# Kernel tuning notes

Hardware: AMD Instinct MI355X
Metric: run time of the kernel (lower is better)

The kernel has to match this reference:

```python
import jax, jax.numpy as jnp
import numpy as np

MARGIN = 0.075
CONF_THRESHOLD = 0.2


def setup_inputs() -> dict:
    key = jax.random.key(0)
    k1, k2, k3 = jax.random.split(key, 3)
    N, D = 32768, 256
    embeddings = jax.random.normal(k1, (N, D), dtype=jnp.float32)
    tags = jax.random.randint(k2, (N,), 0, 500, dtype=jnp.int64)
    confidences = jax.random.uniform(k3, (N,), dtype=jnp.float32)
    return {"embeddings": embeddings, "tags": tags, "confidences": confidences}


def _safe_sqrt(sq):
    # gradient-safe sqrt: zero at sq<=0 (matches d(0)=0, avoids NaN in vjp)
    pos = sq > 0
    return jnp.where(pos, jnp.sqrt(jnp.where(pos, sq, 1.0)), 0.0)


def _triplet_hard_mining(emb, labels):
    n = emb.shape[0]
    # pairwise euclidean distances (cdist p=2)
    sq_norm = jnp.sum(emb * emb, axis=1)  # [n]
    sq = sq_norm[:, None] + sq_norm[None, :] - 2.0 * (emb @ emb.T)
    dist = _safe_sqrt(jnp.maximum(sq, 0.0))  # [n, n]

    same = labels[:, None] == labels[None, :]
    eye = jnp.eye(n, dtype=bool)
    pos_mask = same & ~eye
    neg_mask = ~same

    inf = jnp.float32(jnp.inf)
    hard_pos = jnp.max(jnp.where(pos_mask, dist, -inf), axis=1)  # [n]
    neg_min = jnp.min(jnp.where(neg_mask, dist, inf), axis=1)    # [n]
    # semi-hard negatives: neg dists strictly greater than hardest positive
    shn_mask = neg_mask & (dist > hard_pos[:, None])
    shn_min = jnp.min(jnp.where(shn_mask, dist, inf), axis=1)
    hard_neg = jnp.where(jnp.isfinite(shn_min), shn_min, neg_min)

    valid = jnp.any(pos_mask, axis=1) & jnp.any(neg_mask, axis=1)
    per_anchor = jax.nn.relu(hard_pos - hard_neg + MARGIN)
    per_anchor = jnp.where(valid, per_anchor, 0.0)
    cnt = jnp.sum(valid.astype(jnp.float32))
    # if no valid anchors (also covers <2 unique labels), loss is 0
    return jnp.where(cnt > 0, jnp.sum(per_anchor) / jnp.maximum(cnt, 1.0), 0.0)


def reference(embeddings, tags, confidences):
    n = embeddings.shape[0]
    top_k = int(CONF_THRESHOLD * n)
    _, idx = jax.lax.top_k(confidences, top_k)
    emb = embeddings[idx]
    labels = tags[idx]
    return _triplet_hard_mining(emb, labels)
```

## Files before the change

kernel.cpp:

```cpp
#include <hip/hip_runtime.h>
#include <math.h>

#define D 256
#define MARGIN 0.075f
#define MAXM 96

typedef __bf16 bf8_t __attribute__((ext_vector_type(8)));
typedef float f4_t __attribute__((ext_vector_type(4)));
typedef unsigned long long ull;

#define AS1 __attribute__((address_space(1)))
#define AS3 __attribute__((address_space(3)))
static __device__ __forceinline__ void gload_lds16(const void* g, void* s) {
    __builtin_amdgcn_global_load_lds((const AS1 unsigned int*)g, (AS3 unsigned int*)s, 16, 0, 0);
}

static __device__ __forceinline__ unsigned short f2bf(float x) {
    unsigned u = __float_as_uint(x);
    unsigned r = (u + 0x7fffu + ((u >> 16) & 1u)) >> 16;
    return (unsigned short)r;
}

static __device__ __forceinline__ float dec_min(unsigned cm) {
    return (cm == 0u) ? __builtin_inff() : __uint_as_float(~cm);
}

static __device__ __forceinline__ float rmin16(float v) {
    int s;
    s = __builtin_amdgcn_update_dpp(__float_as_int(v), __float_as_int(v), 0x101, 0xF, 0xF, false);
    v = fminf(v, __int_as_float(s));
    s = __builtin_amdgcn_update_dpp(__float_as_int(v), __float_as_int(v), 0x102, 0xF, 0xF, false);
    v = fminf(v, __int_as_float(s));
    s = __builtin_amdgcn_update_dpp(__float_as_int(v), __float_as_int(v), 0x104, 0xF, 0xF, false);
    v = fminf(v, __int_as_float(s));
    s = __builtin_amdgcn_update_dpp(__float_as_int(v), __float_as_int(v), 0x108, 0xF, 0xF, false);
    v = fminf(v, __int_as_float(s));
    return v;
}

__global__ void k_hist1(const float* __restrict__ conf, int n,
                        unsigned* __restrict__ hist) {
    int i = blockIdx.x * blockDim.x + threadIdx.x;
    if (i < n) atomicAdd(&hist[__float_as_uint(conf[i]) >> 16], 1u);
}

__global__ __launch_bounds__(1024) void k_scan(const unsigned* __restrict__ hist,
                                               unsigned* __restrict__ ctrl, int ksel) {
    __shared__ unsigned part[1024];
    __shared__ int schunk;
    int t = threadIdx.x;
    unsigned k = (unsigned)ksel;
    unsigned s = 0;
    const uint4* h4 = (const uint4*)(hist + t * 64);
    #pragma unroll
    for (int b = 0; b < 16; b++) { uint4 v = h4[b]; s += v.x + v.y + v.z + v.w; }
    part[t] = s;
    __syncthreads();
    for (int off = 1; off < 1024; off <<= 1) {
        unsigned v = (t + off < 1024) ? part[t + off] : 0u;
        __syncthreads();
        part[t] += v;
        __syncthreads();
    }
    if (part[t] >= k && (t == 1023 || part[t + 1] < k)) schunk = t;
    __syncthreads();
    if (t == 0) {
        int c = schunk;
        unsigned cum = (c == 1023) ? 0u : part[c + 1];
        int bin = 0; unsigned rem = 1;
        for (int b = 63; b >= 0; b--) {
            unsigned h = hist[c * 64 + b];
            if (cum + h >= k) { bin = c * 64 + b; rem = k - cum; break; }
            cum += h;
        }
        ctrl[3] = (unsigned)bin;
        ctrl[1] = k - rem;
        ctrl[2] = rem;
    }
}

__global__ void k_sel(const float* __restrict__ conf, int n,
                      unsigned* __restrict__ ctrl, int* __restrict__ idx_sel,
                      ull* __restrict__ cand) {
    int i = blockIdx.x * blockDim.x + threadIdx.x;
    if (i < n) {
        unsigned u = __float_as_uint(conf[i]);
        unsigned t16 = u >> 16, b16 = ctrl[3];
        if (t16 > b16) {
            unsigned pos = atomicAdd(&ctrl[5], 1u);
            idx_sel[pos] = i;
        } else if (t16 == b16) {
            unsigned pos = atomicAdd(&ctrl[6], 1u);
            cand[pos] = ((ull)u << 32) | (unsigned)i;
        }
    }
}

__global__ __launch_bounds__(256) void k_sel2(const unsigned* __restrict__ ctrl,
                                              const ull* __restrict__ cand,
                                              int* __restrict__ idx_sel) {
    int t = threadIdx.x;
    int M = (int)ctrl[6];
    unsigned need = ctrl[2], cgt = ctrl[1];
    for (int j = t; j < M; j += 256) {
        ull cj = cand[j];
        unsigned uj = (unsigned)(cj >> 32);
        unsigned rank = 0;
        for (int m = 0; m < M; m++) {
            ull cm = cand[m];
            unsigned um = (unsigned)(cm >> 32);
            if (um > uj || (um == uj && cm < cj)) rank++;
        }
        if (rank < need) idx_sel[cgt + rank] = (int)(unsigned)(cj & 0xFFFFFFFFu);
    }
}

__global__ void k_gather(const float* __restrict__ emb, const int* __restrict__ tags,
                         const int* __restrict__ idx_sel, int ksel, int np,
                         unsigned short* __restrict__ ebf, float* __restrict__ sqn,
                         int* __restrict__ lsel, unsigned* __restrict__ labhist,
                         int* __restrict__ members) {
    int j = blockIdx.x;
    int t = threadIdx.x;
    if (j < ksel) {
        int src = idx_sel[j];
        float4 v = *(const float4*)&emb[(size_t)src * D + t * 4];
        ushort4 o;
        o.x = f2bf(v.x); o.y = f2bf(v.y); o.z = f2bf(v.z); o.w = f2bf(v.w);
        *(ushort4*)&ebf[(size_t)j * D + t * 4] = o;
        float s = v.x * v.x + v.y * v.y + v.z * v.z + v.w * v.w;
        for (int off = 32; off > 0; off >>= 1) s += __shfl_down(s, off);
        if (t == 0) {
            int lab = tags[src];
            sqn[j] = s; lsel[j] = lab;
            unsigned slot = atomicAdd(&labhist[lab], 1u);
            if (slot < MAXM) members[lab * MAXM + slot] = j;
        }
    } else {
        ushort4 z = {0, 0, 0, 0};
        *(ushort4*)&ebf[(size_t)j * D + t * 4] = z;
        if (t == 0) { sqn[j] = 0.f; lsel[j] = -1; }
    }
}

__global__ __launch_bounds__(256) void k_hardpos(const unsigned short* __restrict__ ebf,
                                                 const float* __restrict__ sqn,
                                                 const int* __restrict__ members,
                                                 const unsigned* __restrict__ labhist,
                                                 unsigned* __restrict__ hp_g) {
    int L = blockIdx.x;
    int t = threadIdx.x;
    int m = (int)labhist[L];
    if (m > MAXM) m = MAXM;
    if (m < 2) return;

    __shared__ unsigned short rows[MAXM * 256];
    __shared__ float lsqn[MAXM];
    __shared__ unsigned hpl[MAXM];
    __shared__ int ridx[MAXM];

    for (int a = t; a < m; a += 256) {
        int r = members[L * MAXM + a];
        ridx[a] = r; lsqn[a] = sqn[r]; hpl[a] = 0u;
    }
    __syncthreads();
    for (int e = t * 8; e < m * 256; e += 256 * 8) {
        int a = e >> 8, c = e & 255;
        *(uint4*)&rows[a * 256 + c] = *(const uint4*)&ebf[(size_t)ridx[a] * D + c];
    }
    __syncthreads();

    int npair = m * (m - 1) / 2;
    for (int pidx = t; pidx < npair; pidx += 256) {
        int a = 0, rem = pidx;
        while (rem >= m - 1 - a) { rem -= m - 1 - a; a++; }
        int b = a + 1 + rem;
        const unsigned* ra = (const unsigned*)&rows[a * 256];
        const unsigned* rb = (const unsigned*)&rows[b * 256];
        float dot = 0.f;
        #pragma unroll 8
        for (int c = 0; c < 128; c++) {
            unsigned ua = ra[c], ub = rb[c];
            float a0 = __uint_as_float(ua << 16);
            float a1 = __uint_as_float(ua & 0xFFFF0000u);
            float b0 = __uint_as_float(ub << 16);
            float b1 = __uint_as_float(ub & 0xFFFF0000u);
            dot = fmaf(a0, b0, dot);
            dot = fmaf(a1, b1, dot);
        }
        float dsq = fmaxf(lsqn[a] + lsqn[b] - 2.f * dot, 0.f);
        unsigned bits = __float_as_uint(dsq);
        atomicMax(&hpl[a], bits);
        atomicMax(&hpl[b], bits);
    }
    __syncthreads();
    for (int a = t; a < m; a += 256) hp_g[ridx[a]] = hpl[a];
}

__global__ __launch_bounds__(256, 3) void k_fused(const unsigned short* __restrict__ Ebf,
                                                  const float* __restrict__ sqn,
                                                  const int* __restrict__ lsel,
                                                  const unsigned* __restrict__ hp_g,
                                                  unsigned* __restrict__ nm_g,
                                                  unsigned* __restrict__ shn_g,
                                                  int np, int nb, int ksel) {
    int rem = blockIdx.x, bi = 0;
    while (rem >= nb - bi) { rem -= nb - bi; bi++; }
    int bj = bi + rem;
    int i0 = bi * 128, j0 = bj * 128;
    bool diag = (bi == bj);

    __shared__ __align__(16) char smem[32768];
    char* ldsA = smem;
    char* ldsB = smem + 16384;

    int t = threadIdx.x;
    int w = t >> 6, l = t & 63;
    int wm = w & 1, wn = w >> 1;
    int lr = l & 15, lq = l >> 4;
    int r7 = lr & 7, rh = lr >> 3;

    int dr = l >> 3;
    int sg = (l & 7) ^ dr;
    const unsigned short* gA = Ebf + (size_t)(i0 + dr) * D + sg * 8;
    const unsigned short* gB = Ebf + (size_t)(j0 + dr) * D + sg * 8;

    f4_t zero = {0.f, 0.f, 0.f, 0.f};
    f4_t acc[4][4];
    #pragma unroll
    for (int p = 0; p < 4; p++)
        #pragma unroll
        for (int q = 0; q < 4; q++) acc[p][q] = zero;

    for (int k0 = 0; k0 < D; k0 += 64) {
        #pragma unroll
        for (int c = 0; c < 4; c++) {
            int R0 = w * 32 + c * 8;
            gload_lds16(gA + (size_t)R0 * D + k0, ldsA + R0 * 128);
            gload_lds16(gB + (size_t)R0 * D + k0, ldsB + R0 * 128);
        }
        __syncthreads();
        #pragma unroll
        for (int ks8 = 0; ks8 < 8; ks8 += 4) {
            bf8_t a[4], b[4];
            #pragma unroll
            for (int p = 0; p < 4; p++) {
                int off = ((wm * 8 + p * 2 + rh) << 10) + ((r7 * 8 + ((ks8 + lq) ^ r7)) << 4);
                a[p] = *(const bf8_t*)(ldsA + off);
            }
            #pragma unroll
            for (int q = 0; q < 4; q++) {
                int off = ((wn * 8 + q * 2 + rh) << 10) + ((r7 * 8 + ((ks8 + lq) ^ r7)) << 4);
                b[q] = *(const bf8_t*)(ldsB + off);
            }
            #pragma unroll
            for (int p = 0; p < 4; p++)
                #pragma unroll
                for (int q = 0; q < 4; q++)
                    acc[p][q] = __builtin_amdgcn_mfma_f32_16x16x32_bf16(a[p], b[q], acc[p][q], 0, 0, 0);
        }
        __syncthreads();
    }

    float* sqnA = (float*)smem;
    float* sqnB = sqnA + 128;
    int* labA = (int*)(sqnB + 128);
    int* labB = labA + 128;
    float* hpA2 = (float*)(labB + 128);
    float* hpB2 = hpA2 + 128;
    if (t < 128) {
        sqnA[t] = sqn[i0 + t];
        labA[t] = lsel[i0 + t];
        hpA2[t] = __uint_as_float(hp_g[i0 + t]);
    } else {
        int u = t - 128;
        sqnB[u] = sqn[j0 + u];
        labB[u] = lsel[j0 + u];
        hpB2[u] = __uint_as_float(hp_g[j0 + u]);
    }
    __syncthreads();

    const float INF = __builtin_inff();
    float dsq[4][4][4];
    int colL[4], ljv[4];
    #pragma unroll
    for (int q = 0; q < 4; q++) { colL[q] = wn * 64 + q * 16 + lr; ljv[q] = labB[colL[q]]; }
    #pragma unroll
    for (int p = 0; p < 4; p++) {
        #pragma unroll
        for (int r = 0; r < 4; r++) {
            int rowL = wm * 64 + p * 16 + lq * 4 + r;
            int gm = i0 + rowL;
            float smi = sqnA[rowL];
            #pragma unroll
            for (int q = 0; q < 4; q++) {
                int gn = j0 + colL[q];
                float s = fmaxf(smi + sqnB[colL[q]] - 2.f * acc[p][q][r], 0.f);
                dsq[p][q][r] = (gm < ksel && gn < ksel) ? s : INF;
            }
        }
    }

    #pragma unroll
    for (int p = 0; p < 4; p++) {
        #pragma unroll
        for (int r = 0; r < 4; r++) {
            int rowL = wm * 64 + p * 16 + lq * 4 + r;
            int li = labA[rowL];
            float hpr = hpA2[rowL];
            float nmv = INF, smv = INF;
            #pragma unroll
            for (int q = 0; q < 4; q++) {
                float d = dsq[p][q][r];
                if (ljv[q] != li) {
                    nmv = fminf(nmv, d);
                    if (d > hpr) smv = fminf(smv, d);
                }
            }
            nmv = rmin16(nmv);
            smv = rmin16(smv);
            if (lr == 0) {
                if (nmv < INF) atomicMax(&nm_g[i0 + rowL], ~__float_as_uint(nmv));
                if (smv < INF) atomicMax(&shn_g[i0 + rowL], ~__float_as_uint(smv));
            }
        }
    }

    if (!diag) {
        #pragma unroll
        for (int q = 0; q < 4; q++) {
            int lj = ljv[q];
            float hpc = hpB2[colL[q]];
            float nmv = INF, smv = INF;
            #pragma unroll
            for (int p = 0; p < 4; p++)
                #pragma unroll
                for (int r = 0; r < 4; r++) {
                    int rowL = wm * 64 + p * 16 + lq * 4 + r;
                    float d = dsq[p][q][r];
                    if (labA[rowL] != lj) {
                        nmv = fminf(nmv, d);
                        if (d > hpc) smv = fminf(smv, d);
                    }
                }
            nmv = fminf(nmv, __shfl_xor(nmv, 16));
            nmv = fminf(nmv, __shfl_xor(nmv, 32));
            smv = fminf(smv, __shfl_xor(smv, 16));
            smv = fminf(smv, __shfl_xor(smv, 32));
            if (lq == 0) {
                if (nmv < INF) atomicMax(&nm_g[j0 + colL[q]], ~__float_as_uint(nmv));
                if (smv < INF) atomicMax(&shn_g[j0 + colL[q]], ~__float_as_uint(smv));
            }
        }
    }
}

__global__ __launch_bounds__(256) void k_loss(const unsigned* __restrict__ hp,
                                              const unsigned* __restrict__ nm,
                                              const unsigned* __restrict__ shn,
                                              const int* __restrict__ lsel,
                                              const unsigned* __restrict__ labhist,
                                              int ksel, float* __restrict__ fsums,
                                              unsigned* __restrict__ ctrl,
                                              float* __restrict__ out) {
    __shared__ float ssum[256], scnt[256];
    int t = threadIdx.x;
    int i = blockIdx.x * 256 + t;
    float sum = 0.f, cnt = 0.f;
    if (i < ksel) {
        int li = lsel[i];
        unsigned h = labhist[li];
        bool valid = (h >= 2u) && ((unsigned)ksel > h);
        float hp2 = __uint_as_float(hp[i]);
        float nm2 = dec_min(nm[i]);
        float sh2 = dec_min(shn[i]);
        float hn2 = isinf(sh2) ? nm2 : sh2;
        float lv = valid ? fmaxf(sqrtf(hp2) - sqrtf(hn2) + MARGIN, 0.f) : 0.f;
        sum = lv;
        cnt = valid ? 1.f : 0.f;
    }
    ssum[t] = sum; scnt[t] = cnt;
    __syncthreads();
    for (int off = 128; off > 0; off >>= 1) {
        if (t < off) { ssum[t] += ssum[t + off]; scnt[t] += scnt[t + off]; }
        __syncthreads();
    }
    if (t == 0) {
        atomicAdd(&fsums[0], ssum[0]);
        atomicAdd(&fsums[1], scnt[0]);
        __threadfence();
        unsigned done = atomicAdd(&ctrl[7], 1u);
        if (done == gridDim.x - 1) {
            float s = atomicAdd(&fsums[0], 0.f);
            float c = atomicAdd(&fsums[1], 0.f);
            out[0] = (c > 0.f) ? (s / fmaxf(c, 1.f)) : 0.f;
        }
    }
}

__global__ void k_wsfail(float* out, float code) { out[0] = code; }

static inline size_t align_up(size_t x, size_t a) { return (x + a - 1) & ~(a - 1); }

extern "C" void kernel_launch(void* const* d_in, const int* in_sizes, int n_in,
                              void* d_out, int out_size, void* d_ws, size_t ws_size,
                              hipStream_t stream) {
    const float* emb  = (const float*)d_in[0];
    const int*   tags = (const int*)d_in[1];
    const float* conf = (const float*)d_in[2];
    float* out = (float*)d_out;

    int n = in_sizes[2];
    int ksel = (int)(0.2 * (double)n);
    int np = ((ksel + 127) / 128) * 128;
    int nb = np / 128;
    int nlab = 512;

    size_t off = 0;
    size_t o_ctrl = off; off = align_up(off + 32 * sizeof(unsigned), 256);
    size_t o_fs   = off; off = align_up(off + 8 * sizeof(float), 256);
    size_t o_lh   = off; off = align_up(off + (size_t)nlab * 4, 256);
    size_t o_hp   = off; off = align_up(off + (size_t)np * 4, 256);
    size_t o_nm   = off; off = align_up(off + (size_t)np * 4, 256);
    size_t o_shn  = off; off = align_up(off + (size_t)np * 4, 256);
    size_t o_h1   = off; off = align_up(off + 65536 * 4, 256);
    size_t zero_bytes = off;
    size_t o_idx  = off; off = align_up(off + (size_t)ksel * 4, 256);
    size_t o_cand = off; off = align_up(off + (size_t)n * 8, 256);
    size_t o_mem  = off; off = align_up(off + (size_t)nlab * MAXM * 4, 256);
    size_t o_lab  = off; off = align_up(off + (size_t)np * 4, 256);
    size_t o_sqn  = off; off = align_up(off + (size_t)np * 4, 256);
    size_t o_ebf  = off; off = align_up(off + (size_t)np * D * 2, 256);

    if (ws_size < off) {
        k_wsfail<<<1, 1, 0, stream>>>(out, -(float)(ws_size >> 20));
        return;
    }

    char* ws = (char*)d_ws;
    unsigned*       ctrl    = (unsigned*)(ws + o_ctrl);
    float*          fsums   = (float*)(ws + o_fs);
    unsigned*       labhist = (unsigned*)(ws + o_lh);
    unsigned*       hp_g    = (unsigned*)(ws + o_hp);
    unsigned*       nm_g    = (unsigned*)(ws + o_nm);
    unsigned*       shn_g   = (unsigned*)(ws + o_shn);
    unsigned*       h1      = (unsigned*)(ws + o_h1);
    int*            idx_sel = (int*)(ws + o_idx);
    ull*            cand    = (ull*)(ws + o_cand);
    int*            members = (int*)(ws + o_mem);
    int*            lsel    = (int*)(ws + o_lab);
    float*          sqn     = (float*)(ws + o_sqn);
    unsigned short* ebf     = (unsigned short*)(ws + o_ebf);

    hipMemsetAsync(d_ws, 0, zero_bytes, stream);
    k_hist1<<<(n + 255) / 256, 256, 0, stream>>>(conf, n, h1);
    k_scan<<<1, 1024, 0, stream>>>(h1, ctrl, ksel);
    k_sel<<<(n + 255) / 256, 256, 0, stream>>>(conf, n, ctrl, idx_sel, cand);
    k_sel2<<<1, 256, 0, stream>>>(ctrl, cand, idx_sel);
    k_gather<<<np, 64, 0, stream>>>(emb, tags, idx_sel, ksel, np, ebf, sqn, lsel,
                                    labhist, members);
    k_hardpos<<<512, 256, 0, stream>>>(ebf, sqn, members, labhist, hp_g);
    int ntri = nb * (nb + 1) / 2;
    k_fused<<<ntri, 256, 0, stream>>>(ebf, sqn, lsel, hp_g, nm_g, shn_g, np, nb, ksel);
    k_loss<<<(ksel + 255) / 256, 256, 0, stream>>>(hp_g, nm_g, shn_g, lsel, labhist,
                                                   ksel, fsums, ctrl, out);
}
```

Measured before the change: 186.2 us.

## Fuse selection kernels via last-block pattern, double-buffer GEMM tiles, fold loss into fused kernel

Merges the histogram and scan kernels, and the select and rank kernels, into single launches where the last block to finish does the serial tail work. The histogram shrinks to a smaller bin range with clamping, and the rank pass stages candidates in LDS. The loss reduction is folded into the end of the pairwise-distance kernel through a last-block counter. The tile loop of the distance GEMM now double-buffers its K tiles in 64KB of LDS, with occupancy lowered from 3 to 2. Padding rows use an infinite squared norm so per-element bounds checks can be dropped. The aim is to cut launch count and idle gaps, at the cost of serial last-block tails and lower occupancy.

```diff
diff --git a/kernel.cpp b/kernel.cpp
--- a/kernel.cpp
+++ b/kernel.cpp
@@ -4,6 +4,7 @@
 #define D 256
 #define MARGIN 0.075f
 #define MAXM 96
+#define NBIN 16384
 
 typedef __bf16 bf8_t __attribute__((ext_vector_type(8)));
 typedef float f4_t __attribute__((ext_vector_type(4)));
@@ -14,6 +15,8 @@
 static __device__ __forceinline__ void gload_lds16(const void* g, void* s) {
     __builtin_amdgcn_global_load_lds((const AS1 unsigned int*)g, (AS3 unsigned int*)s, 16, 0, 0);
 }
+
+#define ALOADU(p) __hip_atomic_load((p), __ATOMIC_RELAXED, __HIP_MEMORY_SCOPE_AGENT)
 
 static __device__ __forceinline__ unsigned short f2bf(float x) {
     unsigned u = __float_as_uint(x);
@@ -38,22 +41,34 @@
     return v;
 }
 
-__global__ void k_hist1(const float* __restrict__ conf, int n,
-                        unsigned* __restrict__ hist) {
-    int i = blockIdx.x * blockDim.x + threadIdx.x;
-    if (i < n) atomicAdd(&hist[__float_as_uint(conf[i]) >> 16], 1u);
-}
-
-__global__ __launch_bounds__(1024) void k_scan(const unsigned* __restrict__ hist,
+__global__ __launch_bounds__(1024) void k_hist(const float* __restrict__ conf, int n,
+                                               unsigned* __restrict__ hist,
                                                unsigned* __restrict__ ctrl, int ksel) {
+    int t = threadIdx.x;
+    int i = blockIdx.x * 1024 + t;
+    if (i < n) {
+        unsigned b = __float_as_uint(conf[i]) >> 16;
+        if (b > NBIN - 1u) b = NBIN - 1u;
+        atomicAdd(&hist[b], 1u);
+    }
+    __threadfence();
+    __syncthreads();
+    __shared__ int lastf;
+    if (t == 0) lastf = (atomicAdd(&ctrl[10], 1u) == gridDim.x - 1) ? 1 : 0;
+    __syncthreads();
+    if (!lastf) return;
+    __threadfence();
+
     __shared__ unsigned part[1024];
     __shared__ int schunk;
-    int t = threadIdx.x;
     unsigned k = (unsigned)ksel;
+    unsigned loc[16];
     unsigned s = 0;
-    const uint4* h4 = (const uint4*)(hist + t * 64);
-    #pragma unroll
-    for (int b = 0; b < 16; b++) { uint4 v = h4[b]; s += v.x + v.y + v.z + v.w; }
+    #pragma unroll
+    for (int b = 0; b < 16; b++) {
+        loc[b] = ALOADU(&hist[t * 16 + b]);
+        s += loc[b];
+    }
     part[t] = s;
     __syncthreads();
     for (int off = 1; off < 1024; off <<= 1) {
@@ -64,13 +79,14 @@
     }
     if (part[t] >= k && (t == 1023 || part[t + 1] < k)) schunk = t;
     __syncthreads();
-    if (t == 0) {
-        int c = schunk;
+    int c = schunk;
+    if (t == c) {
         unsigned cum = (c == 1023) ? 0u : part[c + 1];
         int bin = 0; unsigned rem = 1;
-        for (int b = 63; b >= 0; b--) {
-            unsigned h = hist[c * 64 + b];
-            if (cum + h >= k) { bin = c * 64 + b; rem = k - cum; break; }
+        #pragma unroll
+        for (int b = 15; b >= 0; b--) {
+            unsigned h = loc[b];
+            if (cum + h >= k) { bin = c * 16 + b; rem = k - cum; break; }
             cum += h;
         }
         ctrl[3] = (unsigned)bin;
@@ -79,13 +95,17 @@
     }
 }
 
-__global__ void k_sel(const float* __restrict__ conf, int n,
-                      unsigned* __restrict__ ctrl, int* __restrict__ idx_sel,
-                      ull* __restrict__ cand) {
-    int i = blockIdx.x * blockDim.x + threadIdx.x;
+__global__ __launch_bounds__(1024) void k_sel(const float* __restrict__ conf, int n,
+                                              unsigned* __restrict__ ctrl,
+                                              int* __restrict__ idx_sel,
+                                              ull* __restrict__ cand) {
+    int t = threadIdx.x;
+    int i = blockIdx.x * 1024 + t;
+    unsigned b16 = ctrl[3];
     if (i < n) {
         unsigned u = __float_as_uint(conf[i]);
-        unsigned t16 = u >> 16, b16 = ctrl[3];
+        unsigned t16 = u >> 16;
+        if (t16 > NBIN - 1u) t16 = NBIN - 1u;
         if (t16 > b16) {
             unsigned pos = atomicAdd(&ctrl[5], 1u);
             idx_sel[pos] = i;
@@ -94,34 +114,57 @@
             cand[pos] = ((ull)u << 32) | (unsigned)i;
         }
     }
-}
-
-__global__ __launch_bounds__(256) void k_sel2(const unsigned* __restrict__ ctrl,
-                                              const ull* __restrict__ cand,
-                                              int* __restrict__ idx_sel) {
-    int t = threadIdx.x;
-    int M = (int)ctrl[6];
+    __threadfence();
+    __syncthreads();
+    __shared__ int lastf;
+    if (t == 0) lastf = (atomicAdd(&ctrl[11], 1u) == gridDim.x - 1) ? 1 : 0;
+    __syncthreads();
+    if (!lastf) return;
+    __threadfence();
+
+    __shared__ ull scand[2048];
+    int M = (int)ALOADU(&ctrl[6]);
     unsigned need = ctrl[2], cgt = ctrl[1];
-    for (int j = t; j < M; j += 256) {
-        ull cj = cand[j];
-        unsigned uj = (unsigned)(cj >> 32);
-        unsigned rank = 0;
-        for (int m = 0; m < M; m++) {
-            ull cm = cand[m];
-            unsigned um = (unsigned)(cm >> 32);
-            if (um > uj || (um == uj && cm < cj)) rank++;
-        }
-        if (rank < need) idx_sel[cgt + rank] = (int)(unsigned)(cj & 0xFFFFFFFFu);
-    }
-}
-
-__global__ void k_gather(const float* __restrict__ emb, const int* __restrict__ tags,
-                         const int* __restrict__ idx_sel, int ksel, int np,
-                         unsigned short* __restrict__ ebf, float* __restrict__ sqn,
-                         int* __restrict__ lsel, unsigned* __restrict__ labhist,
-                         int* __restrict__ members) {
-    int j = blockIdx.x;
-    int t = threadIdx.x;
+    if (M <= 2048) {
+        for (int j = t; j < M; j += 1024) scand[j] = ALOADU(&cand[j]);
+        __syncthreads();
+        for (int j = t; j < M; j += 1024) {
+            ull cj = scand[j];
+            unsigned uj = (unsigned)(cj >> 32);
+            unsigned rank = 0;
+            for (int m = 0; m < M; m++) {
+                ull cm = scand[m];
+                unsigned um = (unsigned)(cm >> 32);
+                if (um > uj || (um == uj && cm < cj)) rank++;
+            }
+            if (rank < need) idx_sel[cgt + rank] = (int)(unsigned)(cj & 0xFFFFFFFFu);
+        }
+    } else {
+        for (int j = t; j < M; j += 1024) {
+            ull cj = ALOADU(&cand[j]);
+            unsigned uj = (unsigned)(cj >> 32);
+            unsigned rank = 0;
+            for (int m = 0; m < M; m++) {
+                ull cm = ALOADU(&cand[m]);
+                unsigned um = (unsigned)(cm >> 32);
+                if (um > uj || (um == uj && cm < cj)) rank++;
+            }
+            if (rank < need) idx_sel[cgt + rank] = (int)(unsigned)(cj & 0xFFFFFFFFu);
+        }
+    }
+}
+
+__global__ __launch_bounds__(256) void k_gather(const float* __restrict__ emb,
+                                                const int* __restrict__ tags,
+                                                const int* __restrict__ idx_sel,
+                                                int ksel, int np,
+                                                unsigned short* __restrict__ ebf,
+                                                float* __restrict__ sqn,
+                                                int* __restrict__ lsel,
+                                                unsigned* __restrict__ labhist,
+                                                int* __restrict__ members) {
+    int j = blockIdx.x * 4 + (threadIdx.x >> 6);
+    int t = threadIdx.x & 63;
     if (j < ksel) {
         int src = idx_sel[j];
         float4 v = *(const float4*)&emb[(size_t)src * D + t * 4];
@@ -136,10 +179,10 @@
             unsigned slot = atomicAdd(&labhist[lab], 1u);
             if (slot < MAXM) members[lab * MAXM + slot] = j;
         }
-    } else {
+    } else if (j < np) {
         ushort4 z = {0, 0, 0, 0};
         *(ushort4*)&ebf[(size_t)j * D + t * 4] = z;
-        if (t == 0) { sqn[j] = 0.f; lsel[j] = -1; }
+        if (t == 0) { sqn[j] = __builtin_inff(); lsel[j] = -1; }
     }
 }
 
@@ -197,22 +240,23 @@
     for (int a = t; a < m; a += 256) hp_g[ridx[a]] = hpl[a];
 }
 
-__global__ __launch_bounds__(256, 3) void k_fused(const unsigned short* __restrict__ Ebf,
+__global__ __launch_bounds__(256, 2) void k_fused(const unsigned short* __restrict__ Ebf,
                                                   const float* __restrict__ sqn,
                                                   const int* __restrict__ lsel,
                                                   const unsigned* __restrict__ hp_g,
                                                   unsigned* __restrict__ nm_g,
                                                   unsigned* __restrict__ shn_g,
-                                                  int np, int nb, int ksel) {
+                                                  const unsigned* __restrict__ labhist,
+                                                  unsigned* __restrict__ ctrl,
+                                                  float* __restrict__ out,
+                                                  int np, int nb, int ksel, int ntri) {
     int rem = blockIdx.x, bi = 0;
     while (rem >= nb - bi) { rem -= nb - bi; bi++; }
     int bj = bi + rem;
     int i0 = bi * 128, j0 = bj * 128;
     bool diag = (bi == bj);
 
-    __shared__ __align__(16) char smem[32768];
-    char* ldsA = smem;
-    char* ldsB = smem + 16384;
+    __shared__ __align__(16) char smem[65536];
 
     int t = threadIdx.x;
     int w = t >> 6, l = t & 63;
@@ -232,26 +276,39 @@
         #pragma unroll
         for (int q = 0; q < 4; q++) acc[p][q] = zero;
 
-    for (int k0 = 0; k0 < D; k0 += 64) {
-        #pragma unroll
-        for (int c = 0; c < 4; c++) {
-            int R0 = w * 32 + c * 8;
-            gload_lds16(gA + (size_t)R0 * D + k0, ldsA + R0 * 128);
-            gload_lds16(gB + (size_t)R0 * D + k0, ldsB + R0 * 128);
-        }
+    #pragma unroll
+    for (int c = 0; c < 4; c++) {
+        int R0 = w * 32 + c * 8;
+        gload_lds16(gA + (size_t)R0 * D, smem + R0 * 128);
+        gload_lds16(gB + (size_t)R0 * D, smem + 16384 + R0 * 128);
+    }
+
+    #pragma unroll
+    for (int tt = 0; tt < 4; ++tt) {
+        char* cb = smem + ((tt & 1) << 15);
         __syncthreads();
+        if (tt < 3) {
+            char* nb_ = smem + (((tt + 1) & 1) << 15);
+            int ko = (tt + 1) * 64;
+            #pragma unroll
+            for (int c = 0; c < 4; c++) {
+                int R0 = w * 32 + c * 8;
+                gload_lds16(gA + (size_t)R0 * D + ko, nb_ + R0 * 128);
+                gload_lds16(gB + (size_t)R0 * D + ko, nb_ + 16384 + R0 * 128);
+            }
+        }
         #pragma unroll
         for (int ks8 = 0; ks8 < 8; ks8 += 4) {
             bf8_t a[4], b[4];
             #pragma unroll
             for (int p = 0; p < 4; p++) {
                 int off = ((wm * 8 + p * 2 + rh) << 10) + ((r7 * 8 + ((ks8 + lq) ^ r7)) << 4);
-                a[p] = *(const bf8_t*)(ldsA + off);
+                a[p] = *(const bf8_t*)(cb + off);
             }
             #pragma unroll
             for (int q = 0; q < 4; q++) {
                 int off = ((wn * 8 + q * 2 + rh) << 10) + ((r7 * 8 + ((ks8 + lq) ^ r7)) << 4);
-                b[q] = *(const bf8_t*)(ldsB + off);
+                b[q] = *(const bf8_t*)(cb + 16384 + off);
             }
             #pragma unroll
             for (int p = 0; p < 4; p++)
@@ -259,7 +316,6 @@
                 for (int q = 0; q < 4; q++)
                     acc[p][q] = __builtin_amdgcn_mfma_f32_16x16x32_bf16(a[p], b[q], acc[p][q], 0, 0, 0);
         }
-        __syncthreads();
     }
 
     float* sqnA = (float*)smem;
@@ -283,21 +339,22 @@
     const float INF = __builtin_inff();
     float dsq[4][4][4];
     int colL[4], ljv[4];
-    #pragma unroll
-    for (int q = 0; q < 4; q++) { colL[q] = wn * 64 + q * 16 + lr; ljv[q] = labB[colL[q]]; }
+    float sBv[4];
+    #pragma unroll
+    for (int q = 0; q < 4; q++) {
+        colL[q] = wn * 64 + q * 16 + lr;
+        ljv[q] = labB[colL[q]];
+        sBv[q] = sqnB[colL[q]];
+    }
     #pragma unroll
     for (int p = 0; p < 4; p++) {
         #pragma unroll
         for (int r = 0; r < 4; r++) {
             int rowL = wm * 64 + p * 16 + lq * 4 + r;
-            int gm = i0 + rowL;
             float smi = sqnA[rowL];
             #pragma unroll
-            for (int q = 0; q < 4; q++) {
-                int gn = j0 + colL[q];
-                float s = fmaxf(smi + sqnB[colL[q]] - 2.f * acc[p][q][r], 0.f);
-                dsq[p][q][r] = (gm < ksel && gn < ksel) ? s : INF;
-            }
+            for (int q = 0; q < 4; q++)
+                dsq[p][q][r] = fmaxf(smi + sBv[q] - 2.f * acc[p][q][r], 0.f);
         }
     }
 
@@ -353,32 +410,31 @@
             }
         }
     }
-}
-
-__global__ __launch_bounds__(256) void k_loss(const unsigned* __restrict__ hp,
-                                              const unsigned* __restrict__ nm,
-                                              const unsigned* __restrict__ shn,
-                                              const int* __restrict__ lsel,
-                                              const unsigned* __restrict__ labhist,
-                                              int ksel, float* __restrict__ fsums,
-                                              unsigned* __restrict__ ctrl,
-                                              float* __restrict__ out) {
-    __shared__ float ssum[256], scnt[256];
-    int t = threadIdx.x;
-    int i = blockIdx.x * 256 + t;
+
+    __threadfence();
+    __syncthreads();
+    __shared__ int lastf;
+    if (t == 0) lastf = (atomicAdd(&ctrl[8], 1u) == (unsigned)(ntri - 1)) ? 1 : 0;
+    __syncthreads();
+    if (!lastf) return;
+    __threadfence();
+
     float sum = 0.f, cnt = 0.f;
-    if (i < ksel) {
+    for (int i = t; i < ksel; i += 256) {
         int li = lsel[i];
         unsigned h = labhist[li];
         bool valid = (h >= 2u) && ((unsigned)ksel > h);
-        float hp2 = __uint_as_float(hp[i]);
-        float nm2 = dec_min(nm[i]);
-        float sh2 = dec_min(shn[i]);
-        float hn2 = isinf(sh2) ? nm2 : sh2;
-        float lv = valid ? fmaxf(sqrtf(hp2) - sqrtf(hn2) + MARGIN, 0.f) : 0.f;
-        sum = lv;
-        cnt = valid ? 1.f : 0.f;
-    }
+        if (valid) {
+            float hp2 = __uint_as_float(hp_g[i]);
+            float nm2 = dec_min(ALOADU(&nm_g[i]));
+            float sh2 = dec_min(ALOADU(&shn_g[i]));
+            float hn2 = isinf(sh2) ? nm2 : sh2;
+            sum += fmaxf(sqrtf(hp2) - sqrtf(hn2) + MARGIN, 0.f);
+            cnt += 1.f;
+        }
+    }
+    float* ssum = (float*)smem;
+    float* scnt = ssum + 256;
     ssum[t] = sum; scnt[t] = cnt;
     __syncthreads();
     for (int off = 128; off > 0; off >>= 1) {
@@ -386,15 +442,8 @@
         __syncthreads();
     }
     if (t == 0) {
-        atomicAdd(&fsums[0], ssum[0]);
-        atomicAdd(&fsums[1], scnt[0]);
-        __threadfence();
-        unsigned done = atomicAdd(&ctrl[7], 1u);
-        if (done == gridDim.x - 1) {
-            float s = atomicAdd(&fsums[0], 0.f);
-            float c = atomicAdd(&fsums[1], 0.f);
-            out[0] = (c > 0.f) ? (s / fmaxf(c, 1.f)) : 0.f;
-        }
+        float s = ssum[0], c = scnt[0];
+        out[0] = (c > 0.f) ? (s / fmaxf(c, 1.f)) : 0.f;
     }
 }
 
@@ -418,12 +467,11 @@
 
     size_t off = 0;
     size_t o_ctrl = off; off = align_up(off + 32 * sizeof(unsigned), 256);
-    size_t o_fs   = off; off = align_up(off + 8 * sizeof(float), 256);
     size_t o_lh   = off; off = align_up(off + (size_t)nlab * 4, 256);
     size_t o_hp   = off; off = align_up(off + (size_t)np * 4, 256);
     size_t o_nm   = off; off = align_up(off + (size_t)np * 4, 256);
     size_t o_shn  = off; off = align_up(off + (size_t)np * 4, 256);
-    size_t o_h1   = off; off = align_up(off + 65536 * 4, 256);
+    size_t o_h1   = off; off = align_up(off + (size_t)NBIN * 4, 256);
     size_t zero_bytes = off;
     size_t o_idx  = off; off = align_up(off + (size_t)ksel * 4, 256);
     size_t o_cand = off; off = align_up(off + (size_t)n * 8, 256);
@@ -439,7 +487,6 @@
 
     char* ws = (char*)d_ws;
     unsigned*       ctrl    = (unsigned*)(ws + o_ctrl);
-    float*          fsums   = (float*)(ws + o_fs);
     unsigned*       labhist = (unsigned*)(ws + o_lh);
     unsigned*       hp_g    = (unsigned*)(ws + o_hp);
     unsigned*       nm_g    = (unsigned*)(ws + o_nm);
@@ -453,15 +500,13 @@
     unsigned short* ebf     = (unsigned short*)(ws + o_ebf);
 
     hipMemsetAsync(d_ws, 0, zero_bytes, stream);
-    k_hist1<<<(n + 255) / 256, 256, 0, stream>>>(conf, n, h1);
-    k_scan<<<1, 1024, 0, stream>>>(h1, ctrl, ksel);
-    k_sel<<<(n + 255) / 256, 256, 0, stream>>>(conf, n, ctrl, idx_sel, cand);
-    k_sel2<<<1, 256, 0, stream>>>(ctrl, cand, idx_sel);
-    k_gather<<<np, 64, 0, stream>>>(emb, tags, idx_sel, ksel, np, ebf, sqn, lsel,
-                                    labhist, members);
+    int nhb = (n + 1023) / 1024;
+    k_hist<<<nhb, 1024, 0, stream>>>(conf, n, h1, ctrl, ksel);
+    k_sel<<<nhb, 1024, 0, stream>>>(conf, n, ctrl, idx_sel, cand);
+    k_gather<<<np / 4, 256, 0, stream>>>(emb, tags, idx_sel, ksel, np, ebf, sqn, lsel,
+                                         labhist, members);
     k_hardpos<<<512, 256, 0, stream>>>(ebf, sqn, members, labhist, hp_g);
     int ntri = nb * (nb + 1) / 2;
-    k_fused<<<ntri, 256, 0, stream>>>(ebf, sqn, lsel, hp_g, nm_g, shn_g, np, nb, ksel);
-    k_loss<<<(ksel + 255) / 256, 256, 0, stream>>>(hp_g, nm_g, shn_g, lsel, labhist,
-                                                   ksel, fsums, ctrl, out);
-}
+    k_fused<<<ntri, 256, 0, stream>>>(ebf, sqn, lsel, hp_g, nm_g, shn_g, labhist, ctrl,
+                                      out, np, nb, ksel, ntri);
+}
```

New measurement: 288.8 us. 1.55x slower.
